# Kernel optimization log

Hardware: AMD Instinct MI355X
Metric: run time of the kernel (lower is better)

Reference implementation:

```python
import jax, jax.numpy as jnp
import numpy as np

N_PATCHES = 14
HIDDEN_D = 768
N_HEADS = 12
D_HEAD = HIDDEN_D // N_HEADS
SEQ = N_PATCHES ** 2 + 1  # 197
INPUT_D = 3 * 16 * 16  # c * patch_h * patch_w = 768
LN_EPS = 1e-5


def positional_embeddings(seq_len, d):
    # result[i, j] = sin(i / 10000**(j/d)) if j even else cos(i / 10000**((j-1)/d))
    i = jnp.arange(seq_len, dtype=jnp.float32)[:, None]
    j = jnp.arange(d, dtype=jnp.float32)[None, :]
    even = (jnp.arange(d) % 2 == 0)[None, :]
    denom_even = jnp.power(10000.0, j / d)
    denom_odd = jnp.power(10000.0, (j - 1.0) / d)
    return jnp.where(even, jnp.sin(i / denom_even), jnp.cos(i / denom_odd))


def setup_inputs() -> dict:
    key = jax.random.key(0)
    ks = jax.random.split(key, 12)
    s = 0.02
    return {
        "images": jax.random.normal(ks[0], (128, 3, 224, 224), dtype=jnp.float32),
        "W_map": jax.random.normal(ks[1], (HIDDEN_D, INPUT_D), dtype=jnp.float32) * s,
        "b_map": jax.random.normal(ks[2], (HIDDEN_D,), dtype=jnp.float32) * s,
        "class_token": jax.random.uniform(ks[3], (1, HIDDEN_D), dtype=jnp.float32),
        "ln_w": jnp.ones((SEQ, HIDDEN_D), dtype=jnp.float32),
        "ln_b": jnp.zeros((SEQ, HIDDEN_D), dtype=jnp.float32),
        "Wq": jax.random.normal(ks[4], (N_HEADS, D_HEAD, D_HEAD), dtype=jnp.float32) * s,
        "bq": jax.random.normal(ks[5], (N_HEADS, D_HEAD), dtype=jnp.float32) * s,
        "Wk": jax.random.normal(ks[6], (N_HEADS, D_HEAD, D_HEAD), dtype=jnp.float32) * s,
        "bk": jax.random.normal(ks[7], (N_HEADS, D_HEAD), dtype=jnp.float32) * s,
        "Wv": jax.random.normal(ks[8], (N_HEADS, D_HEAD, D_HEAD), dtype=jnp.float32) * s,
        "bv": jax.random.normal(ks[9], (N_HEADS, D_HEAD), dtype=jnp.float32) * s,
    }


def _forward(images, W_map, b_map, class_token, ln_w, ln_b, Wq, bq, Wk, bk, Wv, bv):
    n = images.shape[0]
    # naive patchify (faithful to source: a plain reshape)
    patches = images.reshape(n, N_PATCHES ** 2, INPUT_D)
    # linear mapper: x @ W.T + b
    tokens = jnp.einsum("npi,di->npd", patches, W_map) + b_map
    # prepend class token
    cls = jnp.broadcast_to(class_token[None], (n, 1, HIDDEN_D))
    tokens = jnp.concatenate([cls, tokens], axis=1)  # [n, SEQ, D]
    # positional embeddings
    tokens = tokens + positional_embeddings(SEQ, HIDDEN_D)[None]
    # LayerNorm over last two dims (SEQ, D) jointly
    mean = jnp.mean(tokens, axis=(-2, -1), keepdims=True)
    var = jnp.var(tokens, axis=(-2, -1), keepdims=True)
    x = (tokens - mean) / jnp.sqrt(var + LN_EPS) * ln_w + ln_b
    # multi-head self-attention (batched over samples and heads)
    xh = x.reshape(n, SEQ, N_HEADS, D_HEAD)  # head-sliced channels
    q = jnp.einsum("bshd,hed->bshe", xh, Wq) + bq[None, None]
    k = jnp.einsum("bshd,hed->bshe", xh, Wk) + bk[None, None]
    v = jnp.einsum("bshd,hed->bshe", xh, Wv) + bv[None, None]
    att = jax.nn.softmax(
        jnp.einsum("bshd,bthd->bhst", q, k) / jnp.sqrt(jnp.float32(D_HEAD)), axis=-1
    )
    msa = jnp.einsum("bhst,bthd->bshd", att, v).reshape(n, SEQ, HIDDEN_D)
    return tokens + msa


def reference(images, W_map, b_map, class_token, ln_w, ln_b, Wq, bq, Wk, bk, Wv, bv):
    return _forward(images, W_map, b_map, class_token, ln_w, ln_b, Wq, bq, Wk, bk, Wv, bv)
```

## Files before the change

### kernel.cpp

```cpp
#include <hip/hip_runtime.h>

typedef float fx4 __attribute__((ext_vector_type(4)));
typedef __bf16 bf16x8 __attribute__((ext_vector_type(8)));
typedef unsigned short ushort8 __attribute__((ext_vector_type(8)));
typedef unsigned int uint2v __attribute__((ext_vector_type(2)));
typedef unsigned int uint4v __attribute__((ext_vector_type(4)));

#define MFMA16(a, b, c) __builtin_amdgcn_mfma_f32_16x16x32_bf16((a), (b), (c), 0, 0, 0)

#if __has_builtin(__builtin_amdgcn_exp2f)
#define EXP2(x) __builtin_amdgcn_exp2f(x)
#else
#define EXP2(x) exp2f(x)
#endif

__device__ __forceinline__ unsigned short f2bf(float f) {
  return __builtin_bit_cast(unsigned short, (__bf16)f);
}

__device__ __forceinline__ ushort8 pack8(fx4 a, fx4 b) {
  ushort8 v;
  v[0] = f2bf(a[0]); v[1] = f2bf(a[1]); v[2] = f2bf(a[2]); v[3] = f2bf(a[3]);
  v[4] = f2bf(b[0]); v[5] = f2bf(b[1]); v[6] = f2bf(b[2]); v[7] = f2bf(b[3]);
  return v;
}

__device__ __forceinline__ uint2v pack2(fx4 v) {
  uint2v r;
  r[0] = (unsigned int)f2bf(v[0]) | ((unsigned int)f2bf(v[1]) << 16);
  r[1] = (unsigned int)f2bf(v[2]) | ((unsigned int)f2bf(v[3]) << 16);
  return r;
}

__device__ __forceinline__ bf16x8 xfrm(uint2v A, uint2v B, int quad, int src0, int src1) {
  uint4v pf;
#pragma unroll
  for (int d = 0; d < 2; d++) {
    int a0 = __shfl((int)A[d], src0, 64);
    int b0 = __shfl((int)B[d], src0, 64);
    pf[d] = (unsigned int)((quad < 2) ? a0 : b0);
    int a1 = __shfl((int)A[d], src1, 64);
    int b1 = __shfl((int)B[d], src1, 64);
    pf[2 + d] = (unsigned int)((quad < 2) ? a1 : b1);
  }
  return __builtin_bit_cast(bf16x8, pf);
}

__device__ __forceinline__ void gl2lds16(const unsigned short* g, void* lds_base) {
  __builtin_amdgcn_global_load_lds(
      (const __attribute__((address_space(1))) void*)(unsigned long long)(g),
      (__attribute__((address_space(3))) void*)(unsigned int)(unsigned long long)(lds_base),
      16, 0, 0);
}

__global__ __launch_bounds__(256) void k_prep(
    const float* __restrict__ img, const float* __restrict__ W,
    const float* __restrict__ Wq, const float* __restrict__ Wk, const float* __restrict__ Wv,
    const float* __restrict__ ct,
    float* __restrict__ pe, unsigned short* __restrict__ imgbf, unsigned short* __restrict__ wbf,
    unsigned short* __restrict__ wqkv,
    float* __restrict__ out, float* __restrict__ sums, float* __restrict__ sqs) {
  const int bid = blockIdx.x, tid = threadIdx.x;
  if (bid < 591) {
    int idx = bid * 256 + tid;
    int s = idx / 768;
    int j = idx - s * 768;
    int jj = j & ~1;
    float ang = (float)s * expf((float)jj * (-9.210340371976184f / 768.0f));
    pe[idx] = (j & 1) ? cosf(ang) : sinf(ang);
  } else if (bid < 10287) {
    size_t i = ((size_t)(bid - 591) * 256 + tid) * 8;
    const float* src;
    unsigned short* dst;
    if (i < 19267584) { src = img + i; dst = imgbf + i; }
    else { size_t j = i - 19267584; src = W + j; dst = wbf + j; }
    const fx4* p = (const fx4*)src;
    *(ushort8*)dst = pack8(p[0], p[1]);
  } else if (bid < 10359) {
    int i = ((bid - 10287) * 256 + tid) * 8;
    const float* src = (i < 49152) ? (Wq + i) : (i < 98304 ? Wk + (i - 49152) : Wv + (i - 98304));
    const fx4* p = (const fx4*)src;
    *(ushort8*)(wqkv + i) = pack8(p[0], p[1]);
  } else {
    const int b = bid - 10359;
    float s = 0.f, q = 0.f;
#pragma unroll
    for (int it = 0; it < 3; it++) {
      int j = tid + it * 256;
      float v = ct[j] + ((j & 1) ? 1.f : 0.f);
      out[(size_t)b * 197 * 768 + j] = v;
      s += v; q += v * v;
    }
    for (int off = 32; off > 0; off >>= 1) { s += __shfl_down(s, off); q += __shfl_down(q, off); }
    __shared__ float rs[4], rq[4];
    int w = tid >> 6;
    if ((tid & 63) == 0) { rs[w] = s; rq[w] = q; }
    __syncthreads();
    if (tid == 0) {
      sums[b] = rs[0] + rs[1] + rs[2] + rs[3];
      sqs[b] = rq[0] + rq[1] + rq[2] + rq[3];
    }
  }
}

__global__ __launch_bounds__(256) void k_tokens(
    const unsigned short* __restrict__ imgbf, const unsigned short* __restrict__ wbf,
    const float* __restrict__ bmap, const float* __restrict__ pe,
    float* __restrict__ out, float* __restrict__ sums, float* __restrict__ sqs) {
  __shared__ __align__(16) ushort8 Sf[16 * 64];
  const int tid = threadIdx.x;
  const int idx = (blockIdx.x & 7) * 147 + (blockIdx.x >> 3);
  const int m0 = (idx / 6) * 128;
  const int n0 = (idx % 6) * 128;
  const int lane = tid & 63;
  const int w = tid >> 6;
  const int quad = lane >> 4, l16 = lane & 15;
  const int m_off = (w & 1) * 64, n_off = (w >> 1) * 64;

  fx4 acc[4][4];
#pragma unroll
  for (int i = 0; i < 4; i++)
#pragma unroll
    for (int j = 0; j < 4; j++) acc[i][j] = (fx4){0.f, 0.f, 0.f, 0.f};

  const unsigned short* pA = imgbf + (size_t)(m0 + w * 16 + l16) * 768 + quad * 8;
  const unsigned short* pB = wbf + (size_t)(n0 + w * 16 + l16) * 768 + quad * 8;
  void* lA0 = (void*)&Sf[(w) * 64];
  void* lA1 = (void*)&Sf[(4 + w) * 64];
  void* lB0 = (void*)&Sf[(8 + w) * 64];
  void* lB1 = (void*)&Sf[(12 + w) * 64];

  for (int k0 = 0; k0 < 768; k0 += 32) {
    __syncthreads();
    gl2lds16(pA + k0, lA0);
    gl2lds16(pA + 64 * 768 + k0, lA1);
    gl2lds16(pB + k0, lB0);
    gl2lds16(pB + 64 * 768 + k0, lB1);
    __syncthreads();
    bf16x8 a[4], b[4];
#pragma unroll
    for (int mt = 0; mt < 4; mt++)
      a[mt] = __builtin_bit_cast(bf16x8, Sf[((w & 1) * 4 + mt) * 64 + lane]);
#pragma unroll
    for (int nt = 0; nt < 4; nt++)
      b[nt] = __builtin_bit_cast(bf16x8, Sf[(8 + (w >> 1) * 4 + nt) * 64 + lane]);
#pragma unroll
    for (int mt = 0; mt < 4; mt++)
#pragma unroll
      for (int nt = 0; nt < 4; nt++) acc[mt][nt] = MFMA16(a[mt], b[nt], acc[mt][nt]);
  }

  float s0 = 0.f, q0 = 0.f, s1 = 0.f, q1 = 0.f;
  const int b0 = m0 / 196;
#pragma unroll
  for (int mt = 0; mt < 4; mt++) {
#pragma unroll
    for (int nt = 0; nt < 4; nt++) {
      const int col = n0 + n_off + nt * 16 + l16;
      const float bc = bmap[col];
#pragma unroll
      for (int r = 0; r < 4; r++) {
        const int gm = m0 + m_off + mt * 16 + quad * 4 + r;
        const int bb = gm / 196;
        const int ss = gm - bb * 196 + 1;
        float val = acc[mt][nt][r] + bc + pe[ss * 768 + col];
        out[((size_t)bb * 197 + ss) * 768 + col] = val;
        if (bb == b0) { s0 += val; q0 += val * val; }
        else          { s1 += val; q1 += val * val; }
      }
    }
  }
  for (int off = 32; off > 0; off >>= 1) {
    s0 += __shfl_down(s0, off); q0 += __shfl_down(q0, off);
    s1 += __shfl_down(s1, off); q1 += __shfl_down(q1, off);
  }
  if (lane == 0) {
    atomicAdd(&sums[b0], s0);
    atomicAdd(&sqs[b0], q0);
    if (b0 + 1 < 128) { atomicAdd(&sums[b0 + 1], s1); atomicAdd(&sqs[b0 + 1], q1); }
  }
}

__global__ __launch_bounds__(512, 2) void k_fused(
    const float* tok, const float* __restrict__ sums, const float* __restrict__ sqs,
    const float* __restrict__ lnw, const float* __restrict__ lnb,
    const unsigned short* __restrict__ wqkv,
    const float* __restrict__ bq, const float* __restrict__ bk, const float* __restrict__ bv,
    float* out) {
  __shared__ __align__(16) ushort8 Kf[26 * 64];
  __shared__ __align__(16) ushort8 Vf[24 * 64];
  __shared__ __align__(16) ushort8 Vt[4 * 32];
  const int tid = threadIdx.x;
  const int bh = blockIdx.x;
  const int b = bh / 12;
  const int h = bh - b * 12;
  const int lane = tid & 63;
  const int w = tid >> 6;
  const int quad = lane >> 4;
  const int l16 = lane & 15;
  const int src0 = l16 + ((quad & 1) << 5);
  const int src1 = src0 + 16;
  const float invN = 1.0f / 151296.0f;
  const float mean = sums[b] * invN;
  const float rstd = rsqrtf(sqs[b] * invN - mean * mean + 1e-5f);
  const int hcol = h * 64;

  bf16x8 qfr[2][2];

  const int jp = w;
  if (jp < 7) {
    bf16x8 wq[4][2], wk[4][2], wv[4][2];
#pragma unroll
    for (int et = 0; et < 4; et++) {
      const int ro = (et * 16 + l16) * 64 + quad * 8;
#pragma unroll
      for (int kk = 0; kk < 2; kk++) {
        wq[et][kk] = *(const bf16x8*)(wqkv + hcol * 64 + ro + kk * 32);
        wk[et][kk] = *(const bf16x8*)(wqkv + 49152 + hcol * 64 + ro + kk * 32);
        wv[et][kk] = *(const bf16x8*)(wqkv + 98304 + hcol * 64 + ro + kk * 32);
      }
    }
    bf16x8 xf[2][2];
#pragma unroll
    for (int s2 = 0; s2 < 2; s2++) {
      const int tt = 2 * jp + s2;
      if (tt < 13) {
        int ss = tt * 16 + l16;
        ss = (ss < 197) ? ss : 196;
#pragma unroll
        for (int kk = 0; kk < 2; kk++) {
          const int col = hcol + kk * 32 + quad * 8;
          const fx4* px = (const fx4*)(tok + (size_t)(b * 197 + ss) * 768 + col);
          const fx4* pw = (const fx4*)(lnw + (size_t)ss * 768 + col);
          const fx4* pb = (const fx4*)(lnb + (size_t)ss * 768 + col);
          fx4 y0 = (px[0] - mean) * rstd * pw[0] + pb[0];
          fx4 y1 = (px[1] - mean) * rstd * pw[1] + pb[1];
          xf[s2][kk] = __builtin_bit_cast(bf16x8, pack8(y0, y1));
        }
        fx4 aq[4], ak[4];
#pragma unroll
        for (int et = 0; et < 4; et++) {
          aq[et] = (fx4){0.f, 0.f, 0.f, 0.f};
          ak[et] = (fx4){0.f, 0.f, 0.f, 0.f};
        }
#pragma unroll
        for (int kk = 0; kk < 2; kk++)
#pragma unroll
          for (int et = 0; et < 4; et++) {
            aq[et] = MFMA16(wq[et][kk], xf[s2][kk], aq[et]);
            ak[et] = MFMA16(wk[et][kk], xf[s2][kk], ak[et]);
          }
        uint2v qp[4], kp[4];
#pragma unroll
        for (int et = 0; et < 4; et++) {
          fx4 bqv = *(const fx4*)(bq + hcol + et * 16 + quad * 4);
          fx4 bkv = *(const fx4*)(bk + hcol + et * 16 + quad * 4);
          qp[et] = pack2((aq[et] + bqv) * 0.18033688f);
          kp[et] = pack2(ak[et] + bkv);
        }
#pragma unroll
        for (int kk = 0; kk < 2; kk++) {
          qfr[s2][kk] = xfrm(qp[2 * kk], qp[2 * kk + 1], quad, src0, src1);
          bf16x8 kfrag = xfrm(kp[2 * kk], kp[2 * kk + 1], quad, src0, src1);
          Kf[(tt * 2 + kk) * 64 + lane] = __builtin_bit_cast(ushort8, kfrag);
        }
      }
    }
    fx4 av[2][4];
#pragma unroll
    for (int s2 = 0; s2 < 2; s2++)
#pragma unroll
      for (int et = 0; et < 4; et++) av[s2][et] = (fx4){0.f, 0.f, 0.f, 0.f};
#pragma unroll
    for (int s2 = 0; s2 < 2; s2++) {
      const int tt = 2 * jp + s2;
      if (tt < 13) {
#pragma unroll
        for (int kk = 0; kk < 2; kk++)
#pragma unroll
          for (int et = 0; et < 4; et++)
            av[s2][et] = MFMA16(xf[s2][kk], wv[et][kk], av[s2][et]);
      }
    }
#pragma unroll
    for (int et = 0; et < 4; et++) {
      const float bvv = bv[hcol + et * 16 + l16];
      fx4 bb4 = (fx4){bvv, bvv, bvv, bvv};
      uint2v v0 = pack2(av[0][et] + bb4);
      uint2v v1 = pack2(av[1][et] + bb4);
      bf16x8 vfrag = xfrm(v0, v1, quad, src0, src1);
      if (jp < 6) Vf[(et * 6 + jp) * 64 + lane] = __builtin_bit_cast(ushort8, vfrag);
      else if (quad < 2) Vt[et * 32 + lane] = __builtin_bit_cast(ushort8, vfrag);
    }
  }
  __syncthreads();

#pragma unroll
  for (int qi = 0; qi < 2; qi++) {
    const int mt = 2 * w + qi;
    if (mt < 13) {
      fx4 sacc[13];
#pragma unroll
      for (int nt = 0; nt < 13; nt++) sacc[nt] = (fx4){0.f, 0.f, 0.f, 0.f};
#pragma unroll
      for (int kk = 0; kk < 2; kk++) {
        bf16x8 qf = qfr[qi][kk];
#pragma unroll
        for (int nt = 0; nt < 13; nt++) {
          bf16x8 kf = __builtin_bit_cast(bf16x8, Kf[(nt * 2 + kk) * 64 + lane]);
          sacc[nt] = MFMA16(kf, qf, sacc[nt]);
        }
      }
      float sm = 0.f;
      uint2v pk[13];
#pragma unroll
      for (int nt = 0; nt < 13; nt++) {
        fx4 p;
#pragma unroll
        for (int r = 0; r < 4; r++) {
          const bool valid = (nt < 12) | (quad * 4 + r < 5);
          p[r] = valid ? EXP2(sacc[nt][r]) : 0.f;
          sm += p[r];
        }
        pk[nt] = pack2(p);
      }
      sm += __shfl_xor(sm, 16);
      sm += __shfl_xor(sm, 32);
      const float inv = 1.0f / sm;

      fx4 oacc[4];
#pragma unroll
      for (int et = 0; et < 4; et++) oacc[et] = (fx4){0.f, 0.f, 0.f, 0.f};
#pragma unroll
      for (int kk = 0; kk < 7; kk++) {
        uint4v pf;
        if (kk < 6) {
          const int nA = 2 * kk, nB = 2 * kk + 1;
#pragma unroll
          for (int d = 0; d < 2; d++) {
            int a0 = __shfl((int)pk[nA][d], src0, 64);
            int b0 = __shfl((int)pk[nB][d], src0, 64);
            pf[d] = (unsigned int)((quad < 2) ? a0 : b0);
            int a1 = __shfl((int)pk[nA][d], src1, 64);
            int b1 = __shfl((int)pk[nB][d], src1, 64);
            pf[2 + d] = (unsigned int)((quad < 2) ? a1 : b1);
          }
        } else {
#pragma unroll
          for (int d = 0; d < 2; d++) {
            int a0 = __shfl((int)pk[12][d], src0, 64);
            pf[d] = (quad < 2) ? (unsigned int)a0 : 0u;
            int a1 = __shfl((int)pk[12][d], src1, 64);
            pf[2 + d] = (quad < 2) ? (unsigned int)a1 : 0u;
          }
        }
        bf16x8 pfrag = __builtin_bit_cast(bf16x8, pf);
#pragma unroll
        for (int et = 0; et < 4; et++) {
          bf16x8 vf;
          if (kk < 6) {
            vf = __builtin_bit_cast(bf16x8, Vf[(et * 6 + kk) * 64 + lane]);
          } else if (quad < 2) {
            vf = __builtin_bit_cast(bf16x8, Vt[et * 32 + lane]);
          } else {
            ushort8 z = {0, 0, 0, 0, 0, 0, 0, 0};
            vf = __builtin_bit_cast(bf16x8, z);
          }
          oacc[et] = MFMA16(vf, pfrag, oacc[et]);
        }
      }
      const int sg = mt * 16 + l16;
      if (sg < 197) {
        float* op = out + ((size_t)b * 197 + sg) * 768 + hcol + quad * 4;
#pragma unroll
        for (int et = 0; et < 4; et++) {
          fx4 cur = *(const fx4*)(op + et * 16);
          cur += oacc[et] * inv;
          *(fx4*)(op + et * 16) = cur;
        }
      }
    }
  }
}

extern "C" void kernel_launch(void* const* d_in, const int* in_sizes, int n_in,
                              void* d_out, int out_size, void* d_ws, size_t ws_size,
                              hipStream_t stream) {
  (void)in_sizes; (void)n_in; (void)out_size; (void)ws_size;
  const float* img  = (const float*)d_in[0];
  const float* Wmap = (const float*)d_in[1];
  const float* bmap = (const float*)d_in[2];
  const float* ct   = (const float*)d_in[3];
  const float* lnw  = (const float*)d_in[4];
  const float* lnb  = (const float*)d_in[5];
  const float* Wq   = (const float*)d_in[6];
  const float* bq   = (const float*)d_in[7];
  const float* Wk   = (const float*)d_in[8];
  const float* bk   = (const float*)d_in[9];
  const float* Wv   = (const float*)d_in[10];
  const float* bv   = (const float*)d_in[11];
  float* out = (float*)d_out;

  float* pe   = (float*)d_ws;
  float* sums = pe + 151296;
  float* sqs  = sums + 128;
  unsigned short* wbf   = (unsigned short*)(sqs + 128);
  unsigned short* imgbf = wbf + 589824;
  unsigned short* wqkv  = imgbf + (size_t)19267584;

  k_prep<<<10487, 256, 0, stream>>>(img, Wmap, Wq, Wk, Wv, ct,
                                    pe, imgbf, wbf, wqkv, out, sums, sqs);
  k_tokens<<<1176, 256, 0, stream>>>(imgbf, wbf, bmap, pe, out, sums, sqs);
  k_fused<<<1536, 512, 0, stream>>>(out, sums, sqs, lnw, lnb, wqkv, bq, bk, bv, out);
}
```

Measured before the change: 349.3 us.

## Fuse image fp32-to-bf16 conversion into the patch-embedding GEMM A-tile load

The prep kernel no longer converts the full image tensor to a bf16 workspace copy. The tokens GEMM now reads fp32 image data straight into registers, prefetching one k-step ahead, and packs it to bf16 as it writes the A tile to LDS. This drops a full write and re-read of a roughly 38 MB bf16 intermediate. In exchange the A operand is fetched at fp32 width, and each image tile is converted once per N-tile block (six times) instead of once in total.

```diff
diff --git a/kernel.cpp b/kernel.cpp
--- a/kernel.cpp
+++ b/kernel.cpp
@@ -54,10 +54,10 @@
 }
 
 __global__ __launch_bounds__(256) void k_prep(
-    const float* __restrict__ img, const float* __restrict__ W,
+    const float* __restrict__ W,
     const float* __restrict__ Wq, const float* __restrict__ Wk, const float* __restrict__ Wv,
     const float* __restrict__ ct,
-    float* __restrict__ pe, unsigned short* __restrict__ imgbf, unsigned short* __restrict__ wbf,
+    float* __restrict__ pe, unsigned short* __restrict__ wbf,
     unsigned short* __restrict__ wqkv,
     float* __restrict__ out, float* __restrict__ sums, float* __restrict__ sqs) {
   const int bid = blockIdx.x, tid = threadIdx.x;
@@ -68,21 +68,17 @@
     int jj = j & ~1;
     float ang = (float)s * expf((float)jj * (-9.210340371976184f / 768.0f));
     pe[idx] = (j & 1) ? cosf(ang) : sinf(ang);
-  } else if (bid < 10287) {
-    size_t i = ((size_t)(bid - 591) * 256 + tid) * 8;
-    const float* src;
-    unsigned short* dst;
-    if (i < 19267584) { src = img + i; dst = imgbf + i; }
-    else { size_t j = i - 19267584; src = W + j; dst = wbf + j; }
-    const fx4* p = (const fx4*)src;
-    *(ushort8*)dst = pack8(p[0], p[1]);
-  } else if (bid < 10359) {
-    int i = ((bid - 10287) * 256 + tid) * 8;
+  } else if (bid < 879) {
+    int i = ((bid - 591) * 256 + tid) * 8;
+    const fx4* p = (const fx4*)(W + i);
+    *(ushort8*)(wbf + i) = pack8(p[0], p[1]);
+  } else if (bid < 951) {
+    int i = ((bid - 879) * 256 + tid) * 8;
     const float* src = (i < 49152) ? (Wq + i) : (i < 98304 ? Wk + (i - 49152) : Wv + (i - 98304));
     const fx4* p = (const fx4*)src;
     *(ushort8*)(wqkv + i) = pack8(p[0], p[1]);
   } else {
-    const int b = bid - 10359;
+    const int b = bid - 951;
     float s = 0.f, q = 0.f;
 #pragma unroll
     for (int it = 0; it < 3; it++) {
@@ -104,7 +100,7 @@
 }
 
 __global__ __launch_bounds__(256) void k_tokens(
-    const unsigned short* __restrict__ imgbf, const unsigned short* __restrict__ wbf,
+    const float* __restrict__ img, const unsigned short* __restrict__ wbf,
     const float* __restrict__ bmap, const float* __restrict__ pe,
     float* __restrict__ out, float* __restrict__ sums, float* __restrict__ sqs) {
   __shared__ __align__(16) ushort8 Sf[16 * 64];
@@ -123,19 +119,28 @@
 #pragma unroll
     for (int j = 0; j < 4; j++) acc[i][j] = (fx4){0.f, 0.f, 0.f, 0.f};
 
-  const unsigned short* pA = imgbf + (size_t)(m0 + w * 16 + l16) * 768 + quad * 8;
+  const float* pA = img + (size_t)(m0 + w * 16 + l16) * 768 + quad * 8;
   const unsigned short* pB = wbf + (size_t)(n0 + w * 16 + l16) * 768 + quad * 8;
-  void* lA0 = (void*)&Sf[(w) * 64];
-  void* lA1 = (void*)&Sf[(4 + w) * 64];
   void* lB0 = (void*)&Sf[(8 + w) * 64];
   void* lB1 = (void*)&Sf[(12 + w) * 64];
 
+  fx4 ra0 = *(const fx4*)(pA + 0);
+  fx4 ra1 = *(const fx4*)(pA + 4);
+  fx4 ra2 = *(const fx4*)(pA + 64 * 768 + 0);
+  fx4 ra3 = *(const fx4*)(pA + 64 * 768 + 4);
+
   for (int k0 = 0; k0 < 768; k0 += 32) {
     __syncthreads();
-    gl2lds16(pA + k0, lA0);
-    gl2lds16(pA + 64 * 768 + k0, lA1);
+    Sf[w * 64 + lane] = pack8(ra0, ra1);
+    Sf[(4 + w) * 64 + lane] = pack8(ra2, ra3);
     gl2lds16(pB + k0, lB0);
     gl2lds16(pB + 64 * 768 + k0, lB1);
+    if (k0 + 32 < 768) {
+      ra0 = *(const fx4*)(pA + k0 + 32);
+      ra1 = *(const fx4*)(pA + k0 + 36);
+      ra2 = *(const fx4*)(pA + 64 * 768 + k0 + 32);
+      ra3 = *(const fx4*)(pA + 64 * 768 + k0 + 36);
+    }
     __syncthreads();
     bf16x8 a[4], b[4];
 #pragma unroll
@@ -404,12 +409,10 @@
   float* pe   = (float*)d_ws;
   float* sums = pe + 151296;
   float* sqs  = sums + 128;
-  unsigned short* wbf   = (unsigned short*)(sqs + 128);
-  unsigned short* imgbf = wbf + 589824;
-  unsigned short* wqkv  = imgbf + (size_t)19267584;
-
-  k_prep<<<10487, 256, 0, stream>>>(img, Wmap, Wq, Wk, Wv, ct,
-                                    pe, imgbf, wbf, wqkv, out, sums, sqs);
-  k_tokens<<<1176, 256, 0, stream>>>(imgbf, wbf, bmap, pe, out, sums, sqs);
+  unsigned short* wbf  = (unsigned short*)(sqs + 128);
+  unsigned short* wqkv = wbf + 589824;
+
+  k_prep<<<1079, 256, 0, stream>>>(Wmap, Wq, Wk, Wv, ct, pe, wbf, wqkv, out, sums, sqs);
+  k_tokens<<<1176, 256, 0, stream>>>(img, wbf, bmap, pe, out, sums, sqs);
   k_fused<<<1536, 512, 0, stream>>>(out, sums, sqs, lnw, lnb, wqkv, bq, bk, bv, out);
 }
```

Measured after the change: 370.0 us. 1.06x slower.
